# Kernel tuning notes

Measured on AMD Instinct MI355X. Metric: run time of the kernel, lower is better.

The kernel has to match this reference:

```python
import jax, jax.numpy as jnp
import numpy as np
import math

STEEPNESS = 10.0
ART_LAMBDA = 0.25
EPS = 1e-10
N = 1024
BATCH = 8


def bitonic_indices(n):
    """Index pairs (a, b) per layer of a bitonic sorting network for n = 2^k.
    Mirrors diffsort's bitonic_network: each layer has n/2 compare-exchange
    pairs; for descending blocks a and b are swapped so that 'min goes to a,
    max goes to b' implements the correct direction."""
    num_blocks = int(math.log2(n))
    assert 2 ** num_blocks == n, 'n must be a power of two'
    layers_a, layers_b = [], []
    for block_idx in range(num_blocks):
        for layer_idx in range(block_idx + 1):
            m = 2 ** (block_idx - layer_idx)
            a_idx, b_idx = [], []
            for i in range(0, n, 2 * m):
                for j in range(m):
                    ix = i + j
                    a, b = ix, ix + m
                    if (ix // 2 ** (block_idx + 1)) % 2 == 1:
                        a, b = b, a
                    a_idx.append(a)
                    b_idx.append(b)
            layers_a.append(a_idx)
            layers_b.append(b_idx)
    return (np.asarray(layers_a, np.int32), np.asarray(layers_b, np.int32))


def setup_inputs() -> dict:
    key = jax.random.key(0)
    vectors = jax.random.normal(key, (BATCH, N), dtype=jnp.float32)
    ia, ib = bitonic_indices(N)
    return {
        'vectors': vectors,
        'idx_a': jnp.asarray(ia),
        'idx_b': jnp.asarray(ib),
    }


def _diffsort(vectors, idx_a, idx_b):
    B, n = vectors.shape
    # Permutation matrix, starts as identity per batch element: [B, n, n]
    X0 = jnp.tile(jnp.eye(n, dtype=vectors.dtype)[None], (B, 1, 1))

    def layer(carry, idx):
        x, X = carry
        ia, ib = idx                     # [k] each, k = n/2, disjoint, cover [0, n)
        a = x[:, ia]                     # [B, k]
        b = x[:, ib]                     # [B, k]
        d = b - a
        # logistic_phi interpolation: sigmoid((b-a) * s / (|a-b| + eps)^lambda)
        alpha = jax.nn.sigmoid(d * STEEPNESS / (jnp.abs(d) + EPS) ** ART_LAMBDA)
        one_m = 1.0 - alpha
        x_min = alpha * a + one_m * b
        x_max = one_m * a + alpha * b
        x = x.at[:, ia].set(x_min).at[:, ib].set(x_max)
        # Update permutation matrix columns (X @ split.T == column gather)
        aX = X[:, :, ia]                 # [B, n, k]
        bX = X[:, :, ib]                 # [B, n, k]
        al = alpha[:, None, :]
        w_min = al * aX + (1.0 - al) * bX
        w_max = (1.0 - al) * aX + al * bX
        X = X.at[:, :, ia].set(w_min).at[:, :, ib].set(w_max)
        return (x, X), None

    (x, X), _ = jax.lax.scan(layer, (vectors, X0), (idx_a, idx_b))
    return x, X


def reference(vectors, idx_a, idx_b):
    # Returns (sorted_vectors [B, n], permutation_matrix [B, n, n])
    return _diffsort(vectors, idx_a, idx_b)
```

## Files before the change

kernel.cpp:

```cpp
#include <hip/hip_runtime.h>
#include <math.h>

#define NN      1024
#define NB      8
#define NLAYERS 55

template<int CTRL>
__device__ __forceinline__ float dpp_xor(float y) {
    int i = __builtin_bit_cast(int, y);
    i = __builtin_amdgcn_update_dpp(i, i, CTRL, 0xF, 0xF, false);
    return __builtin_bit_cast(float, i);
}
template<int OFF>
__device__ __forceinline__ float swz_xor(float y) {
    int i = __builtin_bit_cast(int, y);
    i = __builtin_amdgcn_ds_swizzle(i, OFF);
    return __builtin_bit_cast(float, i);
}
template<int D> __device__ __forceinline__ float lshuf(float y) {
    if constexpr      (D == 1)  return dpp_xor<0xB1>(y);
    else if constexpr (D == 2)  return dpp_xor<0x4E>(y);
    else if constexpr (D == 4)  return swz_xor<0x101F>(y);
    else if constexpr (D == 8)  return swz_xor<0x201F>(y);
    else if constexpr (D == 16) return swz_xor<0x401F>(y);
    else                        return __shfl_xor(y, 32, 64);
}
template<int M> __device__ __forceinline__ float shufp(float y) {
    if constexpr      (M == 4)   return dpp_xor<0xB1>(y);
    else if constexpr (M == 8)   return dpp_xor<0x4E>(y);
    else if constexpr (M == 16)  return swz_xor<0x101F>(y);
    else if constexpr (M == 32)  return swz_xor<0x201F>(y);
    else if constexpr (M == 64)  return swz_xor<0x401F>(y);
    else                         return __shfl_xor(y, 32, 64);
}

__device__ __forceinline__ float bxor(float v, int mask) {
    return __builtin_bit_cast(float, __builtin_bit_cast(int, v) ^ mask);
}
__device__ __forceinline__ float sigm(float d) {
    const float ad = fabsf(d) + 1e-10f;
    const float pw = __expf(-0.25f * __logf(ad));
    const float z  = d * 10.0f * pw;
    return __builtin_amdgcn_rcpf(1.0f + __expf(-z));
}

__device__ __forceinline__ void pairup(float (&x)[4], float (&alv)[4],
                                       int jl, int jh, int sw) {
    const float lo = x[jl], hi = x[jh];
    const float dv = hi - lo;
    const float a  = sigm(bxor(dv, sw << 31));
    alv[jl] = a; alv[jh] = a;
    x[jl] = fmaf(-a, dv, hi);
    x[jh] = fmaf( a, dv, lo);
}
template<int M>
__device__ __forceinline__ void crossup(float (&x)[4], float (&alv)[4],
                                        int c0, int t) {
    constexpr int S = (M==4)?2:(M==8)?3:(M==16)?4:(M==32)?5:(M==64)?6:7;
    const int flip = ((((c0 >> S) & 1) ^ ((c0 >> t) & 1)) << 31);
    #pragma unroll
    for (int j = 0; j < 4; ++j) {
        const float xq = shufp<M>(x[j]);
        const float dv = xq - x[j];
        const float a  = sigm(bxor(dv, flip));
        alv[j] = a;
        x[j]   = fmaf(a, x[j] - xq, xq);
    }
}

__global__ __launch_bounds__(256) void diffsort_alpha4(
    const float* __restrict__ vecs,
    float*       __restrict__ out,
    float*       __restrict__ al_g)
{
    __shared__ float xs[NN];
    const int tid   = threadIdx.x;
    const int batch = blockIdx.x;
    const int c0    = tid * 4;

    float x[4];
    *(float4*)&x[0] = *(const float4*)(vecs + batch * NN + c0);

    float* ap = al_g + (size_t)batch * NLAYERS * NN + c0;

    #pragma unroll 1
    for (int blk = 0; blk < 10; ++blk) {
        #pragma unroll 1
        for (int sub = 0; sub <= blk; ++sub) {
            const int s = blk - sub, t = blk + 1;
            float alv[4];
            switch (s) {
                case 0:
                    pairup(x, alv, 0, 1, ((c0 + 0) >> t) & 1);
                    pairup(x, alv, 2, 3, ((c0 + 2) >> t) & 1);
                    break;
                case 1:
                    pairup(x, alv, 0, 2, ((c0 + 0) >> t) & 1);
                    pairup(x, alv, 1, 3, ((c0 + 1) >> t) & 1);
                    break;
                case 2: crossup<4>  (x, alv, c0, t); break;
                case 3: crossup<8>  (x, alv, c0, t); break;
                case 4: crossup<16> (x, alv, c0, t); break;
                case 5: crossup<32> (x, alv, c0, t); break;
                case 6: crossup<64> (x, alv, c0, t); break;
                case 7: crossup<128>(x, alv, c0, t); break;
                default: {
                    const int m = 1 << s;
                    __syncthreads();
                    *(float4*)&xs[c0] = *(float4*)&x[0];
                    __syncthreads();
                    float xq[4];
                    *(float4*)&xq[0] = *(const float4*)&xs[c0 ^ m];
                    const int flip = ((((c0 >> s) & 1) ^ ((c0 >> t) & 1)) << 31);
                    #pragma unroll
                    for (int j = 0; j < 4; ++j) {
                        const float dv = xq[j] - x[j];
                        const float a  = sigm(bxor(dv, flip));
                        alv[j] = a;
                        x[j]   = fmaf(a, x[j] - xq[j], xq[j]);
                    }
                } break;
            }
            *(float4*)ap = *(float4*)&alv[0];
            ap += NN;
        }
    }

    *(float4*)(out + batch * NN + c0) = *(float4*)&x[0];
}

template<int W64, int DJ>
__device__ __forceinline__ void pairJ(float (&v)[2][16], const float (&al)[16]) {
    #pragma unroll
    for (int r = 0; r < 2; ++r)
        #pragma unroll
        for (int j = 0; j < W64; ++j)
            if ((j & DJ) == 0) {
                const int jl = j, jh = j | DJ;
                const float a  = al[jl];
                const float dv = v[r][jl] - v[r][jh];
                const float lo = v[r][jl];
                v[r][jl] = fmaf( a, dv, v[r][jh]);
                v[r][jh] = fmaf(-a, dv, lo);
            }
}
template<int W64, int D>
__device__ __forceinline__ void laneX(float (&v)[2][16], const float (&al)[16]) {
    #pragma unroll
    for (int r = 0; r < 2; ++r)
        #pragma unroll
        for (int j = 0; j < W64; ++j) {
            const float p = lshuf<D>(v[r][j]);
            v[r][j] = fmaf(al[j], v[r][j] - p, p);
        }
}
template<int W64>
__device__ __forceinline__ void loadA(float (&al)[16], const float* __restrict__ ap) {
    #pragma unroll
    for (int j = 0; j < W64; ++j) al[j] = ap[j * 64];
}

__global__ __launch_bounds__(256) void diffsort_rows3(
    const float* __restrict__ al_g,
    float*       __restrict__ out)
{
    const int tid   = threadIdx.x;
    const int lane  = tid & 63;
    const int wave  = tid >> 6;
    const int batch = blockIdx.x >> 7;
    const int rgrp  = blockIdx.x & 127;
    const int R0    = rgrp * 8 + wave * 2;
    const int WA    = (R0 >> 7) << 7;
    const int W7    = (R0 >> 8) << 8;
    const int W8    = (R0 >> 9) << 9;

    float v[2][16];
    #pragma unroll
    for (int r = 0; r < 2; ++r) {
        const int loc = (R0 + r) & 127;
        v[r][0] = (loc == lane)      ? 1.0f : 0.0f;
        v[r][1] = (loc == lane + 64) ? 1.0f : 0.0f;
    }

    const float* apc = al_g + (size_t)batch * NLAYERS * NN + lane;
    float al[16];

    #define LAX(W64, D)  { loadA<W64>(al, ap); laneX<W64, D>(v, al); ap += NN; }
    #define LPJ(W64, DJ) { loadA<W64>(al, ap); pairJ<W64, DJ>(v, al); ap += NN; }

    const float* ap = apc + WA;
    LAX(2,1)
    LAX(2,2) LAX(2,1)
    LAX(2,4) LAX(2,2) LAX(2,1)
    LAX(2,8) LAX(2,4) LAX(2,2) LAX(2,1)
    LAX(2,16) LAX(2,8) LAX(2,4) LAX(2,2) LAX(2,1)
    LAX(2,32) LAX(2,16) LAX(2,8) LAX(2,4) LAX(2,2) LAX(2,1)
    LPJ(2,1)  LAX(2,32) LAX(2,16) LAX(2,8) LAX(2,4) LAX(2,2) LAX(2,1)

    if (WA & 128) {
        #pragma unroll
        for (int r = 0; r < 2; ++r) {
            v[r][2] = v[r][0]; v[r][3] = v[r][1];
            v[r][0] = 0.0f;    v[r][1] = 0.0f;
        }
    } else {
        #pragma unroll
        for (int r = 0; r < 2; ++r) { v[r][2] = 0.0f; v[r][3] = 0.0f; }
    }
    ap = apc + W7 + 28 * NN;

    LPJ(4,2) LPJ(4,1) LAX(4,32) LAX(4,16) LAX(4,8) LAX(4,4) LAX(4,2) LAX(4,1)

    if (W7 & 256) {
        #pragma unroll
        for (int r = 0; r < 2; ++r) {
            #pragma unroll
            for (int j = 0; j < 4; ++j) { v[r][j+4] = v[r][j]; v[r][j] = 0.0f; }
        }
    } else {
        #pragma unroll
        for (int r = 0; r < 2; ++r)
            #pragma unroll
            for (int j = 4; j < 8; ++j) v[r][j] = 0.0f;
    }
    ap = apc + W8 + 36 * NN;

    LPJ(8,4) LPJ(8,2) LPJ(8,1)
    LAX(8,32) LAX(8,16) LAX(8,8) LAX(8,4) LAX(8,2) LAX(8,1)

    if (W8 & 512) {
        #pragma unroll
        for (int r = 0; r < 2; ++r) {
            #pragma unroll
            for (int j = 0; j < 8; ++j) { v[r][j+8] = v[r][j]; v[r][j] = 0.0f; }
        }
    } else {
        #pragma unroll
        for (int r = 0; r < 2; ++r)
            #pragma unroll
            for (int j = 8; j < 16; ++j) v[r][j] = 0.0f;
    }
    ap = apc + 45 * NN;

    LPJ(16,8) LPJ(16,4) LPJ(16,2) LPJ(16,1)
    LAX(16,32) LAX(16,16) LAX(16,8) LAX(16,4) LAX(16,2) LAX(16,1)

    #undef LAX
    #undef LPJ

    float* Xo = out + (size_t)NB * NN + (size_t)batch * NN * NN;
    #pragma unroll
    for (int r = 0; r < 2; ++r) {
        float* rowp = Xo + (size_t)(R0 + r) * NN + lane;
        #pragma unroll
        for (int j = 0; j < 16; ++j)
            rowp[j * 64] = v[r][j];
    }
}

extern "C" void kernel_launch(void* const* d_in, const int* in_sizes, int n_in,
                              void* d_out, int out_size, void* d_ws, size_t ws_size,
                              hipStream_t stream) {
    const float* vecs = (const float*)d_in[0];
    float*       out  = (float*)d_out;
    float*       al_g = (float*)d_ws;

    diffsort_alpha4<<<NB, 256, 0, stream>>>(vecs, out, al_g);
    diffsort_rows3<<<NB * 128, 256, 0, stream>>>(al_g, out);
}
```

Measured before the change: 102.9 us.

## Interleave alpha workspace layout, double-buffer vector loads, process four rows per wave

The alpha-producing kernel is fully unrolled over its layers and now stores alphas in a lane-interleaved layout, so each lane's K alphas sit contiguously. The row kernel can then fetch them with float2/float4 vector loads and prefetch the next layer into a second register buffer while the current one is applied. Each wave now handles four rows instead of two, halving the grid, and blocks are ordered batch-fastest. The aim is to hide global-load latency and cut redundant alpha traffic. In exchange, register pressure roughly doubles (64 v values plus up to 32 alpha registers), which may lower occupancy.

```diff
diff --git a/kernel.cpp b/kernel.cpp
--- a/kernel.cpp
+++ b/kernel.cpp
@@ -67,8 +67,44 @@
         x[j]   = fmaf(a, x[j] - xq, xq);
     }
 }
-
-__global__ __launch_bounds__(256) void diffsort_alpha4(
+template<int S, int T>
+__device__ __forceinline__ void produce_layer(float (&x)[4], float (&alv)[4],
+                                              int c0, float* xs) {
+    if constexpr (S == 0) {
+        pairup(x, alv, 0, 1, ((c0 + 0) >> T) & 1);
+        pairup(x, alv, 2, 3, ((c0 + 2) >> T) & 1);
+    } else if constexpr (S == 1) {
+        pairup(x, alv, 0, 2, ((c0 + 0) >> T) & 1);
+        pairup(x, alv, 1, 3, ((c0 + 1) >> T) & 1);
+    } else if constexpr (S <= 7) {
+        crossup<(1 << S)>(x, alv, c0, T);
+    } else {
+        constexpr int m = 1 << S;
+        __syncthreads();
+        *(float4*)&xs[c0] = *(float4*)&x[0];
+        __syncthreads();
+        float xq[4];
+        *(float4*)&xq[0] = *(const float4*)&xs[c0 ^ m];
+        const int flip = ((((c0 >> S) & 1) ^ ((c0 >> T) & 1)) << 31);
+        #pragma unroll
+        for (int j = 0; j < 4; ++j) {
+            const float dv = xq[j] - x[j];
+            const float a  = sigm(bxor(dv, flip));
+            alv[j] = a;
+            x[j]   = fmaf(a, x[j] - xq[j], xq[j]);
+        }
+    }
+}
+template<int K>
+__device__ __forceinline__ void storeA(float* slab, int c0, const float (&alv)[4]) {
+    float* p = slab + (c0 & ~(64*K - 1)) + (c0 & 63) * K + ((c0 >> 6) & (K - 1));
+    p[0]   = alv[0];
+    p[K]   = alv[1];
+    p[2*K] = alv[2];
+    p[3*K] = alv[3];
+}
+
+__global__ __launch_bounds__(256) void diffsort_alpha5(
     const float* __restrict__ vecs,
     float*       __restrict__ out,
     float*       __restrict__ al_g)
@@ -81,58 +117,32 @@
     float x[4];
     *(float4*)&x[0] = *(const float4*)(vecs + batch * NN + c0);
 
-    float* ap = al_g + (size_t)batch * NLAYERS * NN + c0;
-
-    #pragma unroll 1
-    for (int blk = 0; blk < 10; ++blk) {
-        #pragma unroll 1
-        for (int sub = 0; sub <= blk; ++sub) {
-            const int s = blk - sub, t = blk + 1;
-            float alv[4];
-            switch (s) {
-                case 0:
-                    pairup(x, alv, 0, 1, ((c0 + 0) >> t) & 1);
-                    pairup(x, alv, 2, 3, ((c0 + 2) >> t) & 1);
-                    break;
-                case 1:
-                    pairup(x, alv, 0, 2, ((c0 + 0) >> t) & 1);
-                    pairup(x, alv, 1, 3, ((c0 + 1) >> t) & 1);
-                    break;
-                case 2: crossup<4>  (x, alv, c0, t); break;
-                case 3: crossup<8>  (x, alv, c0, t); break;
-                case 4: crossup<16> (x, alv, c0, t); break;
-                case 5: crossup<32> (x, alv, c0, t); break;
-                case 6: crossup<64> (x, alv, c0, t); break;
-                case 7: crossup<128>(x, alv, c0, t); break;
-                default: {
-                    const int m = 1 << s;
-                    __syncthreads();
-                    *(float4*)&xs[c0] = *(float4*)&x[0];
-                    __syncthreads();
-                    float xq[4];
-                    *(float4*)&xq[0] = *(const float4*)&xs[c0 ^ m];
-                    const int flip = ((((c0 >> s) & 1) ^ ((c0 >> t) & 1)) << 31);
-                    #pragma unroll
-                    for (int j = 0; j < 4; ++j) {
-                        const float dv = xq[j] - x[j];
-                        const float a  = sigm(bxor(dv, flip));
-                        alv[j] = a;
-                        x[j]   = fmaf(a, x[j] - xq[j], xq[j]);
-                    }
-                } break;
-            }
-            *(float4*)ap = *(float4*)&alv[0];
-            ap += NN;
-        }
-    }
+    float* slab = al_g + (size_t)batch * NLAYERS * NN;
+    float alv[4];
+    #define PL(B, S, K)                                 \
+        produce_layer<S, B + 1>(x, alv, c0, xs);        \
+        storeA<K>(slab, c0, alv);                       \
+        slab += NN;
+    PL(0,0,2)
+    PL(1,1,2) PL(1,0,2)
+    PL(2,2,2) PL(2,1,2) PL(2,0,2)
+    PL(3,3,2) PL(3,2,2) PL(3,1,2) PL(3,0,2)
+    PL(4,4,2) PL(4,3,2) PL(4,2,2) PL(4,1,2) PL(4,0,2)
+    PL(5,5,2) PL(5,4,2) PL(5,3,2) PL(5,2,2) PL(5,1,2) PL(5,0,2)
+    PL(6,6,2) PL(6,5,2) PL(6,4,2) PL(6,3,2) PL(6,2,2) PL(6,1,2) PL(6,0,2)
+    PL(7,7,4) PL(7,6,4) PL(7,5,4) PL(7,4,4) PL(7,3,4) PL(7,2,4) PL(7,1,4) PL(7,0,4)
+    PL(8,8,8) PL(8,7,8) PL(8,6,8) PL(8,5,8) PL(8,4,8) PL(8,3,8) PL(8,2,8) PL(8,1,8) PL(8,0,8)
+    PL(9,9,16) PL(9,8,16) PL(9,7,16) PL(9,6,16) PL(9,5,16)
+    PL(9,4,16) PL(9,3,16) PL(9,2,16) PL(9,1,16) PL(9,0,16)
+    #undef PL
 
     *(float4*)(out + batch * NN + c0) = *(float4*)&x[0];
 }
 
 template<int W64, int DJ>
-__device__ __forceinline__ void pairJ(float (&v)[2][16], const float (&al)[16]) {
-    #pragma unroll
-    for (int r = 0; r < 2; ++r)
+__device__ __forceinline__ void pairJ(float (&v)[4][16], const float (&al)[W64]) {
+    #pragma unroll
+    for (int r = 0; r < 4; ++r)
         #pragma unroll
         for (int j = 0; j < W64; ++j)
             if ((j & DJ) == 0) {
@@ -145,112 +155,149 @@
             }
 }
 template<int W64, int D>
-__device__ __forceinline__ void laneX(float (&v)[2][16], const float (&al)[16]) {
-    #pragma unroll
-    for (int r = 0; r < 2; ++r)
+__device__ __forceinline__ void laneX(float (&v)[4][16], const float (&al)[W64]) {
+    #pragma unroll
+    for (int r = 0; r < 4; ++r)
         #pragma unroll
         for (int j = 0; j < W64; ++j) {
             const float p = lshuf<D>(v[r][j]);
             v[r][j] = fmaf(al[j], v[r][j] - p, p);
         }
 }
-template<int W64>
-__device__ __forceinline__ void loadA(float (&al)[16], const float* __restrict__ ap) {
-    #pragma unroll
-    for (int j = 0; j < W64; ++j) al[j] = ap[j * 64];
-}
-
-__global__ __launch_bounds__(256) void diffsort_rows3(
+__device__ __forceinline__ void ld8(float* d, const float* s) {
+    *(float4*)d       = *(const float4*)s;
+    *(float4*)(d + 4) = *(const float4*)(s + 4);
+}
+__device__ __forceinline__ void ld16(float* d, const float* s) {
+    ld8(d, s); ld8(d + 8, s + 8);
+}
+
+__global__ __launch_bounds__(256) void diffsort_rows4(
     const float* __restrict__ al_g,
     float*       __restrict__ out)
 {
     const int tid   = threadIdx.x;
     const int lane  = tid & 63;
     const int wave  = tid >> 6;
-    const int batch = blockIdx.x >> 7;
-    const int rgrp  = blockIdx.x & 127;
-    const int R0    = rgrp * 8 + wave * 2;
+    const int batch = blockIdx.x & 7;
+    const int rgrp  = blockIdx.x >> 3;
+    const int R0    = rgrp * 16 + wave * 4;
     const int WA    = (R0 >> 7) << 7;
     const int W7    = (R0 >> 8) << 8;
     const int W8    = (R0 >> 9) << 9;
 
-    float v[2][16];
-    #pragma unroll
-    for (int r = 0; r < 2; ++r) {
+    float v[4][16];
+    #pragma unroll
+    for (int r = 0; r < 4; ++r) {
         const int loc = (R0 + r) & 127;
         v[r][0] = (loc == lane)      ? 1.0f : 0.0f;
         v[r][1] = (loc == lane + 64) ? 1.0f : 0.0f;
-    }
-
-    const float* apc = al_g + (size_t)batch * NLAYERS * NN + lane;
-    float al[16];
-
-    #define LAX(W64, D)  { loadA<W64>(al, ap); laneX<W64, D>(v, al); ap += NN; }
-    #define LPJ(W64, DJ) { loadA<W64>(al, ap); pairJ<W64, DJ>(v, al); ap += NN; }
-
-    const float* ap = apc + WA;
-    LAX(2,1)
-    LAX(2,2) LAX(2,1)
-    LAX(2,4) LAX(2,2) LAX(2,1)
-    LAX(2,8) LAX(2,4) LAX(2,2) LAX(2,1)
-    LAX(2,16) LAX(2,8) LAX(2,4) LAX(2,2) LAX(2,1)
-    LAX(2,32) LAX(2,16) LAX(2,8) LAX(2,4) LAX(2,2) LAX(2,1)
-    LPJ(2,1)  LAX(2,32) LAX(2,16) LAX(2,8) LAX(2,4) LAX(2,2) LAX(2,1)
+        #pragma unroll
+        for (int j = 2; j < 16; ++j) v[r][j] = 0.0f;
+    }
+
+    const float* baseg = al_g + (size_t)batch * NLAYERS * NN;
+
+    {
+        const float* apA = baseg + WA + lane * 2;
+        float alA[2], alB[2];
+        *(float2*)alA = *(const float2*)apA;
+        #define AX(CUR, NXT, D, LAST) do {                                    \
+            if (!(LAST)) *(float2*)(NXT) = *(const float2*)(apA + NN);        \
+            laneX<2, D>(v, CUR);  apA += NN; } while (0);
+        #define AJ(CUR, NXT, DJ, LAST) do {                                   \
+            if (!(LAST)) *(float2*)(NXT) = *(const float2*)(apA + NN);        \
+            pairJ<2, DJ>(v, CUR); apA += NN; } while (0);
+        AX(alA, alB, 1, 0)
+        AX(alB, alA, 2, 0) AX(alA, alB, 1, 0)
+        AX(alB, alA, 4, 0) AX(alA, alB, 2, 0) AX(alB, alA, 1, 0)
+        AX(alA, alB, 8, 0) AX(alB, alA, 4, 0) AX(alA, alB, 2, 0) AX(alB, alA, 1, 0)
+        AX(alA, alB,16, 0) AX(alB, alA, 8, 0) AX(alA, alB, 4, 0) AX(alB, alA, 2, 0)
+        AX(alA, alB, 1, 0)
+        AX(alB, alA,32, 0) AX(alA, alB,16, 0) AX(alB, alA, 8, 0) AX(alA, alB, 4, 0)
+        AX(alB, alA, 2, 0) AX(alA, alB, 1, 0)
+        AJ(alB, alA, 1, 0) AX(alA, alB,32, 0) AX(alB, alA,16, 0) AX(alA, alB, 8, 0)
+        AX(alB, alA, 4, 0) AX(alA, alB, 2, 0) AX(alB, alA, 1, 1)
+        #undef AX
+        #undef AJ
+    }
 
     if (WA & 128) {
         #pragma unroll
-        for (int r = 0; r < 2; ++r) {
+        for (int r = 0; r < 4; ++r) {
             v[r][2] = v[r][0]; v[r][3] = v[r][1];
             v[r][0] = 0.0f;    v[r][1] = 0.0f;
         }
-    } else {
-        #pragma unroll
-        for (int r = 0; r < 2; ++r) { v[r][2] = 0.0f; v[r][3] = 0.0f; }
-    }
-    ap = apc + W7 + 28 * NN;
-
-    LPJ(4,2) LPJ(4,1) LAX(4,32) LAX(4,16) LAX(4,8) LAX(4,4) LAX(4,2) LAX(4,1)
+    }
+
+    {
+        const float* apB = baseg + 28 * NN + W7 + lane * 4;
+        float alC[4], alD[4];
+        *(float4*)alC = *(const float4*)apB;
+        #define BX(CUR, NXT, D, LAST) do {                                    \
+            if (!(LAST)) *(float4*)(NXT) = *(const float4*)(apB + NN);        \
+            laneX<4, D>(v, CUR);  apB += NN; } while (0);
+        #define BJ(CUR, NXT, DJ, LAST) do {                                   \
+            if (!(LAST)) *(float4*)(NXT) = *(const float4*)(apB + NN);        \
+            pairJ<4, DJ>(v, CUR); apB += NN; } while (0);
+        BJ(alC, alD, 2, 0) BJ(alD, alC, 1, 0)
+        BX(alC, alD,32, 0) BX(alD, alC,16, 0) BX(alC, alD, 8, 0) BX(alD, alC, 4, 0)
+        BX(alC, alD, 2, 0) BX(alD, alC, 1, 1)
+        #undef BX
+        #undef BJ
+    }
 
     if (W7 & 256) {
         #pragma unroll
-        for (int r = 0; r < 2; ++r) {
+        for (int r = 0; r < 4; ++r)
             #pragma unroll
             for (int j = 0; j < 4; ++j) { v[r][j+4] = v[r][j]; v[r][j] = 0.0f; }
-        }
-    } else {
-        #pragma unroll
-        for (int r = 0; r < 2; ++r)
-            #pragma unroll
-            for (int j = 4; j < 8; ++j) v[r][j] = 0.0f;
-    }
-    ap = apc + W8 + 36 * NN;
-
-    LPJ(8,4) LPJ(8,2) LPJ(8,1)
-    LAX(8,32) LAX(8,16) LAX(8,8) LAX(8,4) LAX(8,2) LAX(8,1)
+    }
+
+    {
+        const float* apC = baseg + 36 * NN + W8 + lane * 8;
+        float alE[8], alF[8];
+        ld8(alE, apC);
+        #define CX(CUR, NXT, D, LAST) do {                                    \
+            if (!(LAST)) ld8(NXT, apC + NN);                                  \
+            laneX<8, D>(v, CUR);  apC += NN; } while (0);
+        #define CJ(CUR, NXT, DJ, LAST) do {                                   \
+            if (!(LAST)) ld8(NXT, apC + NN);                                  \
+            pairJ<8, DJ>(v, CUR); apC += NN; } while (0);
+        CJ(alE, alF, 4, 0) CJ(alF, alE, 2, 0) CJ(alE, alF, 1, 0)
+        CX(alF, alE,32, 0) CX(alE, alF,16, 0) CX(alF, alE, 8, 0) CX(alE, alF, 4, 0)
+        CX(alF, alE, 2, 0) CX(alE, alF, 1, 1)
+        #undef CX
+        #undef CJ
+    }
 
     if (W8 & 512) {
         #pragma unroll
-        for (int r = 0; r < 2; ++r) {
+        for (int r = 0; r < 4; ++r)
             #pragma unroll
             for (int j = 0; j < 8; ++j) { v[r][j+8] = v[r][j]; v[r][j] = 0.0f; }
-        }
-    } else {
-        #pragma unroll
-        for (int r = 0; r < 2; ++r)
-            #pragma unroll
-            for (int j = 8; j < 16; ++j) v[r][j] = 0.0f;
-    }
-    ap = apc + 45 * NN;
-
-    LPJ(16,8) LPJ(16,4) LPJ(16,2) LPJ(16,1)
-    LAX(16,32) LAX(16,16) LAX(16,8) LAX(16,4) LAX(16,2) LAX(16,1)
-
-    #undef LAX
-    #undef LPJ
+    }
+
+    {
+        const float* apD = baseg + 45 * NN + lane * 16;
+        float alG[16], alH[16];
+        ld16(alG, apD);
+        #define DX(CUR, NXT, D, LAST) do {                                    \
+            if (!(LAST)) ld16(NXT, apD + NN);                                 \
+            laneX<16, D>(v, CUR);  apD += NN; } while (0);
+        #define DJ_(CUR, NXT, DJ, LAST) do {                                  \
+            if (!(LAST)) ld16(NXT, apD + NN);                                 \
+            pairJ<16, DJ>(v, CUR); apD += NN; } while (0);
+        DJ_(alG, alH, 8, 0) DJ_(alH, alG, 4, 0) DJ_(alG, alH, 2, 0) DJ_(alH, alG, 1, 0)
+        DX(alG, alH,32, 0) DX(alH, alG,16, 0) DX(alG, alH, 8, 0) DX(alH, alG, 4, 0)
+        DX(alG, alH, 2, 0) DX(alH, alG, 1, 1)
+        #undef DX
+        #undef DJ_
+    }
 
     float* Xo = out + (size_t)NB * NN + (size_t)batch * NN * NN;
     #pragma unroll
-    for (int r = 0; r < 2; ++r) {
+    for (int r = 0; r < 4; ++r) {
         float* rowp = Xo + (size_t)(R0 + r) * NN + lane;
         #pragma unroll
         for (int j = 0; j < 16; ++j)
@@ -265,6 +312,6 @@
     float*       out  = (float*)d_out;
     float*       al_g = (float*)d_ws;
 
-    diffsort_alpha4<<<NB, 256, 0, stream>>>(vecs, out, al_g);
-    diffsort_rows3<<<NB * 128, 256, 0, stream>>>(al_g, out);
-}
+    diffsort_alpha5<<<NB, 256, 0, stream>>>(vecs, out, al_g);
+    diffsort_rows4<<<NB * 64, 256, 0, stream>>>(al_g, out);
+}
```

Measured after the change: 108.0 us. +4.9%, slower.
